# Kernel optimization log

Hardware: AMD Instinct MI355X
Metric: run time of the kernel (lower is better)

Reference implementation:

```python
import jax, jax.numpy as jnp
import numpy as np

B, T, D = 4, 4096, 64

def setup_inputs() -> dict:
    key = jax.random.key(0)
    k1, k2, k3 = jax.random.split(key, 3)
    x = jax.random.normal(k1, (B, T, D), dtype=jnp.float32)
    # att_dense1 kernel (zeros init in source; use small random for a meaningful baseline)
    W1 = jax.random.normal(k2, (D, D), dtype=jnp.float32) * 0.05
    b1 = jnp.zeros((D,), dtype=jnp.float32)
    # att_dense2 kernel: glorot_normal
    W2 = jax.random.normal(k3, (D, D), dtype=jnp.float32) * jnp.sqrt(2.0 / (D + D))
    b2 = jnp.zeros((D,), dtype=jnp.float32)
    return {"x": x, "W1": W1, "b1": b1, "W2": W2, "b2": b2}

def reference(x, W1, b1, W2, b2):
    # Per-timestep MLP: Dense(D, softmax) -> Dense(D, tanh)
    h1 = jax.nn.softmax(jnp.einsum('btd,de->bte', x, W1) + b1, axis=-1)
    encoded = jnp.tanh(jnp.einsum('btd,de->bte', h1, W2) + b2)  # [B,T,D]
    # scores[b,i,j] = <x[b,i], encoded[b,j]>
    scores = jnp.einsum('bid,bjd->bij', x, encoded)             # [B,T,T]
    attention = jax.nn.softmax(scores, axis=-1)
    # K.permute_dimensions(attention,(0,2,1)) then batch_dot with x:
    # out[b,i,d] = sum_j attention[b,j,i] * x[b,j,d]
    return jnp.einsum('bji,bjd->bid', attention, x)             # [B,T,D]
```

## Files before the change

### kernel.cpp

```cpp
#include <hip/hip_runtime.h>


typedef _Float16 f16;
typedef __attribute__((ext_vector_type(8))) _Float16 f16x8;
typedef __attribute__((ext_vector_type(4))) _Float16 f16x4;
typedef __attribute__((ext_vector_type(4))) float f32x4;

#define TT 4096
#define BB 4
#define BT (BB*TT)
#define SPLIT_A 16

#define MFMA32(A,B,C) __builtin_amdgcn_mfma_f32_16x16x32_f16(A,B,C,0,0,0)
#define MFMA16(A,B,C) __builtin_amdgcn_mfma_f32_16x16x16f16(A,B,C,0,0,0)

#if __has_builtin(__builtin_amdgcn_exp2f)
#define EXP2F(x) __builtin_amdgcn_exp2f(x)
#else
#define EXP2F(x) exp2f(x)
#endif

#define LOG2E 1.4426950408889634f

__global__ __launch_bounds__(256, 1) void k_encode(
    const float* __restrict__ x,
    const float* __restrict__ W1, const float* __restrict__ W2,
    const float* __restrict__ b1, const float* __restrict__ b2,
    f16* __restrict__ ench,
    f16* __restrict__ xafh, f16* __restrict__ xtf,
    float* __restrict__ Zbuf) {
  __shared__ float xS[4][16][68];
  __shared__ float encS[4][16][68];
  int tid = threadIdx.x;
  int w = tid >> 6, lane = tid & 63, quad = lane >> 4, l15 = lane & 15;
  if (tid < 64) Zbuf[blockIdx.x * 64 + tid] = 0.f;
  int slice = blockIdx.x * 4 + w;
  int base = slice * 16;
  f16x8 w1h[4][2], w1l[4][2];
#pragma unroll
  for (int mt = 0; mt < 4; ++mt)
#pragma unroll
    for (int kc = 0; kc < 2; ++kc) {
      f16 h8[8], l8[8];
#pragma unroll
      for (int t = 0; t < 8; ++t) {
        float v = W1[(size_t)(kc * 32 + quad * 8 + t) * 64 + mt * 16 + l15];
        f16 h = (f16)v;
        h8[t] = h; l8[t] = (f16)(v - (float)h);
      }
      w1h[mt][kc] = *(f16x8*)h8;
      w1l[mt][kc] = *(f16x8*)l8;
    }
  f16x4 w2h[4][4], w2l[4][4];
#pragma unroll
  for (int mt = 0; mt < 4; ++mt)
#pragma unroll
    for (int kt = 0; kt < 4; ++kt) {
      f16 h4[4], l4[4];
#pragma unroll
      for (int t = 0; t < 4; ++t) {
        float v = W2[(size_t)(kt * 16 + quad * 4 + t) * 64 + mt * 16 + l15];
        f16 h = (f16)v;
        h4[t] = h; l4[t] = (f16)(v - (float)h);
      }
      w2h[mt][kt] = *(f16x4*)h4;
      w2l[mt][kt] = *(f16x4*)l4;
    }
  f16x8 xbh[2], xbl[2];
#pragma unroll
  for (int kc = 0; kc < 2; ++kc) {
    const float4* p = (const float4*)(x + (size_t)(base + l15) * 64 + kc * 32 + quad * 8);
    float4 v0 = p[0], v1 = p[1];
    float v[8] = {v0.x, v0.y, v0.z, v0.w, v1.x, v1.y, v1.z, v1.w};
    f16 h8[8], l8[8];
#pragma unroll
    for (int t = 0; t < 8; ++t) {
      f16 h = (f16)v[t];
      h8[t] = h; l8[t] = (f16)(v[t] - (float)h);
    }
    xbh[kc] = *(f16x8*)h8;
    xbl[kc] = *(f16x8*)l8;
    size_t off = (size_t)slice * 1024 + kc * 512 + quad * 128 + l15 * 8;
    *(f16x8*)(xafh + off) = xbh[kc];
    *(float4*)&xS[w][l15][kc * 32 + quad * 8] = v0;
    *(float4*)&xS[w][l15][kc * 32 + quad * 8 + 4] = v1;
  }
  f32x4 acc1[4];
#pragma unroll
  for (int mt = 0; mt < 4; ++mt) {
    f32x4 z = {0.f, 0.f, 0.f, 0.f};
    acc1[mt] = z;
  }
#pragma unroll
  for (int kc = 0; kc < 2; ++kc)
#pragma unroll
    for (int mt = 0; mt < 4; ++mt) {
      acc1[mt] = MFMA32(w1h[mt][kc], xbh[kc], acc1[mt]);
      acc1[mt] = MFMA32(w1h[mt][kc], xbl[kc], acc1[mt]);
      acc1[mt] = MFMA32(w1l[mt][kc], xbh[kc], acc1[mt]);
    }
  float h1[4][4];
#pragma unroll
  for (int mt = 0; mt < 4; ++mt) {
    float4 bv = *(const float4*)(b1 + mt * 16 + quad * 4);
    h1[mt][0] = acc1[mt][0] + bv.x;
    h1[mt][1] = acc1[mt][1] + bv.y;
    h1[mt][2] = acc1[mt][2] + bv.z;
    h1[mt][3] = acc1[mt][3] + bv.w;
  }
  float m1 = h1[0][0];
#pragma unroll
  for (int mt = 0; mt < 4; ++mt)
#pragma unroll
    for (int r = 0; r < 4; ++r) m1 = fmaxf(m1, h1[mt][r]);
  m1 = fmaxf(m1, __shfl_xor(m1, 16));
  m1 = fmaxf(m1, __shfl_xor(m1, 32));
  float ssum = 0.f;
  float ev[4][4];
#pragma unroll
  for (int mt = 0; mt < 4; ++mt)
#pragma unroll
    for (int r = 0; r < 4; ++r) {
      ev[mt][r] = EXP2F((h1[mt][r] - m1) * LOG2E);
      ssum += ev[mt][r];
    }
  ssum += __shfl_xor(ssum, 16);
  ssum += __shfl_xor(ssum, 32);
  float rs = __builtin_amdgcn_rcpf(ssum);
  f16x4 p1h[4], p1l[4];
#pragma unroll
  for (int mt = 0; mt < 4; ++mt)
#pragma unroll
    for (int r = 0; r < 4; ++r) {
      float p = ev[mt][r] * rs;
      f16 h = (f16)p;
      p1h[mt][r] = h;
      p1l[mt][r] = (f16)(p - (float)h);
    }
  f32x4 acc2[4];
#pragma unroll
  for (int mt = 0; mt < 4; ++mt) {
    f32x4 z = {0.f, 0.f, 0.f, 0.f};
    acc2[mt] = z;
  }
#pragma unroll
  for (int kt = 0; kt < 4; ++kt)
#pragma unroll
    for (int mt = 0; mt < 4; ++mt) {
      acc2[mt] = MFMA16(w2h[mt][kt], p1h[kt], acc2[mt]);
      acc2[mt] = MFMA16(w2h[mt][kt], p1l[kt], acc2[mt]);
      acc2[mt] = MFMA16(w2l[mt][kt], p1h[kt], acc2[mt]);
    }
#pragma unroll
  for (int mt = 0; mt < 4; ++mt) {
    float4 bv = *(const float4*)(b2 + mt * 16 + quad * 4);
    float bb[4] = {bv.x, bv.y, bv.z, bv.w};
    float o4[4];
#pragma unroll
    for (int r = 0; r < 4; ++r) {
      float hv = acc2[mt][r] + bb[r];
      float ex = EXP2F(hv * (2.0f * LOG2E));
      float th = 1.0f - 2.0f * __builtin_amdgcn_rcpf(ex + 1.0f);
      o4[r] = th * LOG2E;
    }
    *(float4*)&encS[w][l15][mt * 16 + quad * 4] = *(float4*)o4;
  }
#pragma unroll
  for (int k = 0; k < 2; ++k) {
    int e = k * 64 + lane;
    int n = e & 15, quad2 = (e >> 4) & 3, kc = e >> 6;
    const float4* p = (const float4*)&encS[w][n][kc * 32 + quad2 * 8];
    float4 v0 = p[0], v1 = p[1];
    float v[8] = {v0.x, v0.y, v0.z, v0.w, v1.x, v1.y, v1.z, v1.w};
    f16 h8[8];
#pragma unroll
    for (int t = 0; t < 8; ++t) h8[t] = (f16)v[t];
    *(f16x8*)(ench + ((size_t)slice * 128 + e) * 8) = *(f16x8*)h8;
  }
  int b = slice >> 8, ls = slice & 255;
#pragma unroll
  for (int k = 0; k < 4; ++k) {
    f16 p4[4];
#pragma unroll
    for (int t = 0; t < 4; ++t) p4[t] = (f16)xS[w][k * 4 + t][lane];
    size_t off = ((((size_t)b * (TT / 16) + ls) * 4 + k) * 64 + lane) * 4;
    *(f16x4*)(xtf + off) = *(f16x4*)p4;
  }
}

__global__ __launch_bounds__(512, 4) void k_statsM(
    const f16* __restrict__ xafh, const f16* __restrict__ ench,
    float* __restrict__ Zbuf) {
  int tid = threadIdx.x;
  int w = tid >> 6, lane = tid & 63, quad = lane >> 4, l15 = lane & 15;
  int jb = blockIdx.x * 256 + w * 32;
  int b = jb >> 12;
  f16x8 xa[2][2];
#pragma unroll
  for (int mt = 0; mt < 2; ++mt)
#pragma unroll
    for (int kc = 0; kc < 2; ++kc) {
      size_t off = (size_t)((jb >> 4) + mt) * 1024 + kc * 512 + quad * 128 + l15 * 8;
      xa[mt][kc] = *(const f16x8*)(xafh + off);
    }
  float l_run[8];
#pragma unroll
  for (int s = 0; s < 8; ++s) l_run[s] = 0.f;
  int i0 = blockIdx.y * (TT / SPLIT_A);
  size_t ebase = (size_t)((b * TT + i0) >> 4) * 1024 + quad * 128 + l15 * 8;
  const f16* pEh = ench + ebase;
  for (int it = 0; it < TT / SPLIT_A / 64; ++it) {
    f32x4 acc[2][4];
#pragma unroll
    for (int mt = 0; mt < 2; ++mt)
#pragma unroll
      for (int nt = 0; nt < 4; ++nt) {
        f32x4 z = {0.f, 0.f, 0.f, 0.f};
        acc[mt][nt] = z;
      }
#pragma unroll
    for (int kc = 0; kc < 2; ++kc) {
      f16x8 ebf[4];
#pragma unroll
      for (int nt = 0; nt < 4; ++nt)
        ebf[nt] = *(const f16x8*)(pEh + nt * 1024 + kc * 512);
#pragma unroll
      for (int mt = 0; mt < 2; ++mt)
#pragma unroll
        for (int nt = 0; nt < 4; ++nt)
          acc[mt][nt] = MFMA32(xa[mt][kc], ebf[nt], acc[mt][nt]);
    }
#pragma unroll
    for (int mt = 0; mt < 2; ++mt)
#pragma unroll
      for (int r = 0; r < 4; ++r)
        l_run[mt * 4 + r] += EXP2F(acc[mt][0][r]) + EXP2F(acc[mt][1][r]) +
                             EXP2F(acc[mt][2][r]) + EXP2F(acc[mt][3][r]);
    pEh += 4096;
  }
#pragma unroll
  for (int s = 0; s < 8; ++s) {
    float l = l_run[s];
#pragma unroll
    for (int off = 1; off < 16; off <<= 1) l += __shfl_xor(l, off);
    l_run[s] = l;
  }
  if (l15 == 0) {
#pragma unroll
    for (int mt = 0; mt < 2; ++mt)
#pragma unroll
      for (int r = 0; r < 4; ++r)
        atomicAdd(Zbuf + jb + mt * 16 + quad * 4 + r, l_run[mt * 4 + r]);
  }
}

#define OUTB_STEP(CAH, NAH)                                                  \
  {                                                                          \
    f16x4 pvh[4];                                                            \
    _Pragma("unroll") for (int mtb = 0; mtb < 4; ++mtb)                      \
        pvh[mtb] = *(const f16x4*)(pPV + mtb * 64);                          \
    float4 zv = *(const float4*)pZ;                                          \
    float rz[4];                                                             \
    rz[0] = __builtin_amdgcn_rcpf(zv.x);                                     \
    rz[1] = __builtin_amdgcn_rcpf(zv.y);                                     \
    rz[2] = __builtin_amdgcn_rcpf(zv.z);                                     \
    rz[3] = __builtin_amdgcn_rcpf(zv.w);                                     \
    NAH[0] = *(const f16x8*)(pAh);     NAH[1] = *(const f16x8*)(pAh + 512);  \
    f32x4 sacc[2];                                                           \
    _Pragma("unroll") for (int kc = 0; kc < 2; ++kc)                         \
      _Pragma("unroll") for (int nt = 0; nt < 2; ++nt)                       \
          sacc[nt] = MFMA32(CAH[kc], ebr[nt][kc], kc == 0 ? kzero : sacc[nt]); \
    f16x4 pbh[2];                                                            \
    _Pragma("unroll") for (int nt = 0; nt < 2; ++nt)                         \
      _Pragma("unroll") for (int r = 0; r < 4; ++r)                          \
          pbh[nt][r] = (f16)(EXP2F(sacc[nt][r]) * rz[r]);                    \
    _Pragma("unroll") for (int mtb = 0; mtb < 4; ++mtb)                      \
      _Pragma("unroll") for (int nt = 0; nt < 2; ++nt)                       \
          oacc[nt][mtb] = MFMA16(pbh[nt], pvh[mtb], oacc[nt][mtb]);          \
    pAh += 1024; pPV += 1024; pZ += 16;                                      \
  }

__global__ __launch_bounds__(512, 4) void k_outB(
    const f16* __restrict__ xafh, const f16* __restrict__ xtf,
    const f16* __restrict__ ench,
    const float* __restrict__ Zv, float* __restrict__ slabs, int jlen) {
  int tid = threadIdx.x;
  int w = tid >> 6, lane = tid & 63, quad = lane >> 4, l15 = lane & 15;
  int ibase = blockIdx.x * 256;
  int iw = ibase + w * 32;
  int b = ibase >> 12;
  f16x8 ebr[2][2];
#pragma unroll
  for (int nt = 0; nt < 2; ++nt)
#pragma unroll
    for (int kc = 0; kc < 2; ++kc) {
      size_t off = (size_t)((iw >> 4) + nt) * 1024 + kc * 512 + quad * 128 + l15 * 8;
      ebr[nt][kc] = *(const f16x8*)(ench + off);
    }
  f32x4 oacc[2][4];
#pragma unroll
  for (int nt = 0; nt < 2; ++nt)
#pragma unroll
    for (int mtb = 0; mtb < 4; ++mtb) {
      f32x4 z = {0.f, 0.f, 0.f, 0.f};
      oacc[nt][mtb] = z;
    }
  const f32x4 kzero = {0.f, 0.f, 0.f, 0.f};
  int jt0 = blockIdx.y * jlen;
  int nit = jlen / 16;
  size_t jf0 = (size_t)b * TT + jt0;
  const f16* pAh = xafh + (jf0 >> 4) * 1024 + quad * 128 + l15 * 8;
  const f16* pPV = xtf + ((size_t)b * (TT / 16) + (jt0 >> 4)) * 1024 +
                   quad * 256 + l15 * 4;
  const float* pZ = Zv + jf0 + quad * 4;
  f16x8 cah[2], nah[2];
  cah[0] = *(const f16x8*)(pAh);       cah[1] = *(const f16x8*)(pAh + 512);
  pAh += 1024;
  for (int t = 0; t < nit; t += 2) {
    OUTB_STEP(cah, nah)
    OUTB_STEP(nah, cah)
  }
  float* slab = slabs + (size_t)blockIdx.y * BT * 64;
#pragma unroll
  for (int nt = 0; nt < 2; ++nt)
#pragma unroll
    for (int r = 0; r < 4; ++r) {
      int i = iw + nt * 16 + quad * 4 + r;
#pragma unroll
      for (int mtb = 0; mtb < 4; ++mtb)
        slab[(size_t)i * 64 + mtb * 16 + l15] = oacc[nt][mtb][r];
    }
}

__global__ __launch_bounds__(256) void k_reduce(const float* __restrict__ slabs,
                                                float* __restrict__ out,
                                                int nsplit) {
  int e = (blockIdx.x * 256 + threadIdx.x) * 4;
  float4 acc = *(const float4*)(slabs + e);
  for (int s = 1; s < nsplit; ++s) {
    float4 v = *(const float4*)(slabs + (size_t)s * BT * 64 + e);
    acc.x += v.x; acc.y += v.y; acc.z += v.z; acc.w += v.w;
  }
  *(float4*)(out + e) = acc;
}

extern "C" void kernel_launch(void* const* d_in, const int* in_sizes, int n_in,
                              void* d_out, int out_size, void* d_ws,
                              size_t ws_size, hipStream_t stream) {
  const float* x = (const float*)d_in[0];
  const float* W1 = (const float*)d_in[1];
  const float* b1 = (const float*)d_in[2];
  const float* W2 = (const float*)d_in[3];
  const float* b2 = (const float*)d_in[4];
  float* out = (float*)d_out;

  f16* xafh = (f16*)d_ws;
  f16* xafl = xafh + (size_t)BT * 64;
  f16* xtf  = xafl + (size_t)BT * 64;
  f16* ench = xtf + (size_t)BT * 128;
  f16* encl = ench + (size_t)BT * 64;
  float* Zv = (float*)(encl + (size_t)BT * 64);
  f16* w1fh = (f16*)(Zv + BT);
  f16* w1fl = w1fh + 4096;
  f16* w2fh = w1fl + 4096;
  f16* w2fl = w2fh + 4096;
  float* slabs = (float*)(w2fl + 4096);

  size_t base_bytes = (size_t)((char*)slabs - (char*)d_ws);
  size_t slab_bytes = (size_t)BT * 64 * sizeof(float);
  int nsplit = 8;
  while (nsplit > 1 && base_bytes + (size_t)nsplit * slab_bytes > ws_size)
    nsplit >>= 1;

  k_encode<<<dim3(BT / 64), dim3(256), 0, stream>>>(
      x, W1, W2, b1, b2, ench, xafh, xtf, Zv);
  k_statsM<<<dim3(BT / 256, SPLIT_A), dim3(512), 0, stream>>>(xafh, ench, Zv);
  k_outB<<<dim3(BT / 256, nsplit), dim3(512), 0, stream>>>(
      xafh, xtf, ench, Zv, slabs, TT / nsplit);
  k_reduce<<<dim3(BT * 64 / 1024), dim3(256), 0, stream>>>(slabs, out, nsplit);
}
```

Measured before the change: 118.3 us.

## Stage shared A and PV tiles in double-buffered LDS in k_outB

All eight waves in a k_outB block previously loaded the same A and PV tiles from global memory on every j-step. Now 256 threads load each 16-row tile once per block into a double-buffered shared-memory buffer, and all waves read their MFMA operands from it. The next tile is prefetched into registers while the current one is computed. This is meant to cut redundant global and L1 traffic, but it adds a __syncthreads on every short iteration. The prefetch of tile t+1 on the last iteration also reads one tile past the block's range.

```diff
diff --git a/kernel.cpp b/kernel.cpp
--- a/kernel.cpp
+++ b/kernel.cpp
@@ -254,36 +254,12 @@
   }
 }
 
-#define OUTB_STEP(CAH, NAH)                                                  \
-  {                                                                          \
-    f16x4 pvh[4];                                                            \
-    _Pragma("unroll") for (int mtb = 0; mtb < 4; ++mtb)                      \
-        pvh[mtb] = *(const f16x4*)(pPV + mtb * 64);                          \
-    float4 zv = *(const float4*)pZ;                                          \
-    float rz[4];                                                             \
-    rz[0] = __builtin_amdgcn_rcpf(zv.x);                                     \
-    rz[1] = __builtin_amdgcn_rcpf(zv.y);                                     \
-    rz[2] = __builtin_amdgcn_rcpf(zv.z);                                     \
-    rz[3] = __builtin_amdgcn_rcpf(zv.w);                                     \
-    NAH[0] = *(const f16x8*)(pAh);     NAH[1] = *(const f16x8*)(pAh + 512);  \
-    f32x4 sacc[2];                                                           \
-    _Pragma("unroll") for (int kc = 0; kc < 2; ++kc)                         \
-      _Pragma("unroll") for (int nt = 0; nt < 2; ++nt)                       \
-          sacc[nt] = MFMA32(CAH[kc], ebr[nt][kc], kc == 0 ? kzero : sacc[nt]); \
-    f16x4 pbh[2];                                                            \
-    _Pragma("unroll") for (int nt = 0; nt < 2; ++nt)                         \
-      _Pragma("unroll") for (int r = 0; r < 4; ++r)                          \
-          pbh[nt][r] = (f16)(EXP2F(sacc[nt][r]) * rz[r]);                    \
-    _Pragma("unroll") for (int mtb = 0; mtb < 4; ++mtb)                      \
-      _Pragma("unroll") for (int nt = 0; nt < 2; ++nt)                       \
-          oacc[nt][mtb] = MFMA16(pbh[nt], pvh[mtb], oacc[nt][mtb]);          \
-    pAh += 1024; pPV += 1024; pZ += 16;                                      \
-  }
-
 __global__ __launch_bounds__(512, 4) void k_outB(
     const f16* __restrict__ xafh, const f16* __restrict__ xtf,
     const f16* __restrict__ ench,
     const float* __restrict__ Zv, float* __restrict__ slabs, int jlen) {
+  __shared__ f16 sA[2][1024];
+  __shared__ f16 sPV[2][1024];
   int tid = threadIdx.x;
   int w = tid >> 6, lane = tid & 63, quad = lane >> 4, l15 = lane & 15;
   int ibase = blockIdx.x * 256;
@@ -309,16 +285,55 @@
   int jt0 = blockIdx.y * jlen;
   int nit = jlen / 16;
   size_t jf0 = (size_t)b * TT + jt0;
-  const f16* pAh = xafh + (jf0 >> 4) * 1024 + quad * 128 + l15 * 8;
-  const f16* pPV = xtf + ((size_t)b * (TT / 16) + (jt0 >> 4)) * 1024 +
-                   quad * 256 + l15 * 4;
+  const f16* gA  = xafh + (jf0 >> 4) * 1024;
+  const f16* gPV = xtf + ((size_t)b * (TT / 16) + (jt0 >> 4)) * 1024;
   const float* pZ = Zv + jf0 + quad * 4;
-  f16x8 cah[2], nah[2];
-  cah[0] = *(const f16x8*)(pAh);       cah[1] = *(const f16x8*)(pAh + 512);
-  pAh += 1024;
-  for (int t = 0; t < nit; t += 2) {
-    OUTB_STEP(cah, nah)
-    OUTB_STEP(nah, cah)
+  bool doA = tid < 128, doPV = tid >= 128 && tid < 256;
+  int sidx = doA ? tid * 8 : (tid - 128) * 8;
+  {
+    f16x8 st;
+    if (doA)  st = *(const f16x8*)(gA + sidx);
+    if (doPV) st = *(const f16x8*)(gPV + sidx);
+    if (doA)  *(f16x8*)&sA[0][sidx] = st;
+    if (doPV) *(f16x8*)&sPV[0][sidx] = st;
+  }
+  __syncthreads();
+  for (int t = 0; t < nit; ++t) {
+    int cur = t & 1;
+    f16x8 st;
+    if (doA)  st = *(const f16x8*)(gA + (size_t)(t + 1) * 1024 + sidx);
+    if (doPV) st = *(const f16x8*)(gPV + (size_t)(t + 1) * 1024 + sidx);
+    f16x8 ca0 = *(const f16x8*)&sA[cur][quad * 128 + l15 * 8];
+    f16x8 ca1 = *(const f16x8*)&sA[cur][512 + quad * 128 + l15 * 8];
+    float4 zv = *(const float4*)pZ;
+    float rz[4];
+    rz[0] = __builtin_amdgcn_rcpf(zv.x);
+    rz[1] = __builtin_amdgcn_rcpf(zv.y);
+    rz[2] = __builtin_amdgcn_rcpf(zv.z);
+    rz[3] = __builtin_amdgcn_rcpf(zv.w);
+    f32x4 sacc[2];
+#pragma unroll
+    for (int nt = 0; nt < 2; ++nt) {
+      sacc[nt] = MFMA32(ca0, ebr[nt][0], kzero);
+      sacc[nt] = MFMA32(ca1, ebr[nt][1], sacc[nt]);
+    }
+    f16x4 pbh[2];
+#pragma unroll
+    for (int nt = 0; nt < 2; ++nt)
+#pragma unroll
+      for (int r = 0; r < 4; ++r)
+        pbh[nt][r] = (f16)(EXP2F(sacc[nt][r]) * rz[r]);
+#pragma unroll
+    for (int mtb = 0; mtb < 4; ++mtb) {
+      f16x4 pvh = *(const f16x4*)&sPV[cur][quad * 256 + mtb * 64 + l15 * 4];
+#pragma unroll
+      for (int nt = 0; nt < 2; ++nt)
+        oacc[nt][mtb] = MFMA16(pbh[nt], pvh, oacc[nt][mtb]);
+    }
+    if (doA)  *(f16x8*)&sA[cur ^ 1][sidx] = st;
+    if (doPV) *(f16x8*)&sPV[cur ^ 1][sidx] = st;
+    pZ += 16;
+    __syncthreads();
   }
   float* slab = slabs + (size_t)blockIdx.y * BT * 64;
 #pragma unroll
```

Result: no change. 116.2 us (-1.8%).
